# Kernel optimization log

Hardware: AMD Instinct MI355X
Metric: run time of the kernel (lower is better)

Reference implementation:

```python
import jax, jax.numpy as jnp
import numpy as np

B, N, D, H = 4, 2048, 64, 8

def setup_inputs() -> dict:
    key = jax.random.key(0)
    ks = jax.random.split(key, 6)
    s = 0.05
    return {
        "x":  jax.random.normal(ks[0], (B, N, D), dtype=jnp.float32),
        "Wq": jax.random.normal(ks[1], (D, D * H), dtype=jnp.float32) * s,
        "Wk": jax.random.normal(ks[2], (D, D * H), dtype=jnp.float32) * s,
        "Wv": jax.random.normal(ks[3], (D, D * H), dtype=jnp.float32) * s,
        "Wu": jax.random.normal(ks[4], (D * H, D), dtype=jnp.float32) * s,
        "bu": jnp.zeros((D,), dtype=jnp.float32),
    }

def reference(x, Wq, Wk, Wv, Wu, bu):
    b, n, d = x.shape
    h = Wq.shape[1] // d
    # projections: each head has full width d (per the original module)
    q = (x @ Wq).reshape(b, n, h, d).transpose(0, 2, 1, 3)  # [b,h,n,d]
    k = (x @ Wk).reshape(b, n, h, d).transpose(0, 2, 1, 3)
    v = (x @ Wv).reshape(b, n, h, d).transpose(0, 2, 1, 3)
    scores = jnp.einsum('bhnd,bhmd->bhnm', q, k) / jnp.sqrt(jnp.float32(d))
    w = jax.nn.softmax(scores, axis=-1)
    y = jnp.einsum('bhnm,bhmd->bhnd', w, v)          # [b,h,n,d]
    y = y.transpose(0, 2, 1, 3).reshape(b, n, h * d)  # [b,n,h*d]
    return y @ Wu + bu
```

## Files before the change

kernel.cpp:

```cpp
#include <hip/hip_runtime.h>
#include <hip/hip_bf16.h>

#define BB 4
#define NN 2048
#define DD 64
#define HH 8
#define DHH 512

typedef __bf16 bf16_t;
typedef __bf16 bf16x8 __attribute__((ext_vector_type(8)));
typedef __bf16 bf16x4 __attribute__((ext_vector_type(4)));
typedef float f32x4 __attribute__((ext_vector_type(4)));
typedef long long i64;
typedef i64 i64x2 __attribute__((ext_vector_type(2)));
typedef _Float16 f16_t;
typedef _Float16 f16x4 __attribute__((ext_vector_type(4)));
typedef __fp16 h16x2 __attribute__((ext_vector_type(2)));

__device__ __forceinline__ void dma16(const void* g, void* l) {
    __builtin_amdgcn_global_load_lds(
        (const __attribute__((address_space(1))) unsigned int*)g,
        (__attribute__((address_space(3))) unsigned int*)l,
        16, 0, 0);
}

#define MFMA   __builtin_amdgcn_mfma_f32_16x16x32_bf16
#define MFMA8  __builtin_amdgcn_mfma_f32_16x16x32_fp8_fp8
#define MFMA16F __builtin_amdgcn_mfma_f32_16x16x16f16

#define QSCALE 0.18033688011112042f


__global__ __launch_bounds__(256) void prep(
    const float* __restrict__ Wq, const float* __restrict__ Wk,
    const float* __restrict__ Wv, const float* __restrict__ Wu,
    bf16_t* __restrict__ Wqt, bf16_t* __restrict__ Wkt,
    bf16_t* __restrict__ Wvt, bf16_t* __restrict__ Wut)
{
    const int bid = blockIdx.x, tid = threadIdx.x;
    if (bid < 12) {
        const int m = bid >> 2, slice = bid & 3;
        const float* src = (m == 0) ? Wq : (m == 1) ? Wk : Wv;
        bf16_t* dst = (m == 0) ? Wqt : (m == 1) ? Wkt : Wvt;
        const float scale = (m == 0) ? QSCALE : 1.0f;
        const int dc = slice * 128 + (tid >> 1);
        const int kbase = (tid & 1) * 32;
        #pragma unroll
        for (int k0 = 0; k0 < 4; ++k0) {
            bf16x8 p;
            #pragma unroll
            for (int j = 0; j < 8; ++j)
                p[j] = (bf16_t)(src[(size_t)(kbase + k0 * 8 + j) * 512 + dc] * scale);
            *(bf16x8*)(dst + dc * 64 + kbase + k0 * 8) = p;
        }
    } else {
        const int kq = (bid - 12) * 128;
        const int dc = tid >> 2, sub = (tid & 3) * 32;
        #pragma unroll
        for (int k0 = 0; k0 < 4; ++k0) {
            bf16x8 p;
            #pragma unroll
            for (int j = 0; j < 8; ++j)
                p[j] = (bf16_t)Wu[(size_t)(kq + sub + k0 * 8 + j) * 64 + dc];
            *(bf16x8*)(Wut + dc * 512 + kq + sub + k0 * 8) = p;
        }
    }
}

__global__ __launch_bounds__(256) void qkv_mfma(
    const float* __restrict__ x, const bf16_t* __restrict__ Wqt,
    const bf16_t* __restrict__ Wkt, const bf16_t* __restrict__ Wvt,
    char* __restrict__ q8, char* __restrict__ k8, f16_t* __restrict__ vt)
{
    const int n0   = blockIdx.x * 64;
    const int h    = blockIdx.y;
    const int tid  = threadIdx.x;
    const int w    = tid >> 6;
    const int lane = tid & 63;
    const int quad = lane >> 4;
    const int c    = lane & 15;
    const int cq   = c & 7;
    const int l8   = lane >> 3;
    const int lg   = (lane & 7) ^ l8;
    const int lo   = l8 * 128 + lg * 16;
    const int sw0  = ((quad    ) ^ cq) * 16;
    const int sw1  = ((quad + 4) ^ cq) * 16;
    const int w2048 = w * 2048;

    __shared__ __align__(16) float  xs[64 * 64];
    __shared__ __align__(16) bf16_t Wqs[64 * 64], Wks[64 * 64], Wvs[64 * 64];

    {
        const int rloc = lane >> 4;
        const int s    = lane & 15;
        #pragma unroll
        for (int j = 0; j < 4; ++j) {
            int chunk = w * 4 + j;
            int r7 = (chunk * 4 + rloc) & 7;
            const char* src = (const char*)(x + (size_t)(n0 + chunk * 4 + rloc) * 64)
                            + ((s & 8) | ((s & 7) ^ r7)) * 16;
            dma16(src, (char*)xs + chunk * 1024);
        }
    }
    const char* qg = (const char*)Wqt + (size_t)h * 8192;
    const char* kg = (const char*)Wkt + (size_t)h * 8192;
    const char* vg = (const char*)Wvt + (size_t)h * 8192;
    dma16(qg + w2048 + lo,        (char*)Wqs + w2048);
    dma16(qg + w2048 + 1024 + lo, (char*)Wqs + w2048 + 1024);
    dma16(kg + w2048 + lo,        (char*)Wks + w2048);
    dma16(kg + w2048 + 1024 + lo, (char*)Wks + w2048 + 1024);
    dma16(vg + w2048 + lo,        (char*)Wvs + w2048);
    dma16(vg + w2048 + 1024 + lo, (char*)Wvs + w2048 + 1024);
    __syncthreads();

    auto xfrag = [&](int row, int kk) -> bf16x8 {
        const char* rbase = (const char*)xs + row * 256;
        int g0 = kk * 8 + ((quad * 2    ) ^ cq);
        int g1 = kk * 8 + ((quad * 2 + 1) ^ cq);
        f32x4 a = *(const f32x4*)(rbase + g0 * 16);
        f32x4 b = *(const f32x4*)(rbase + g1 * 16);
        bf16x8 r;
        r[0] = (bf16_t)a[0]; r[1] = (bf16_t)a[1]; r[2] = (bf16_t)a[2]; r[3] = (bf16_t)a[3];
        r[4] = (bf16_t)b[0]; r[5] = (bf16_t)b[1]; r[6] = (bf16_t)b[2]; r[7] = (bf16_t)b[3];
        return r;
    };

    bf16x8 xf0 = xfrag(w * 16 + c, 0);
    bf16x8 xf1 = xfrag(w * 16 + c, 1);

    const int gr = n0 + w * 16 + c;
    const int bb = gr >> 11, nn = gr & 2047;
    char* qrow_g = q8 + (((size_t)bb * HH + h) * NN + nn) * 64;
    char* krow_g = k8 + (((size_t)bb * HH + h) * NN + nn) * 64;
    const int nsw = nn & 3;

    #pragma unroll
    for (int mb = 0; mb < 4; ++mb) {
        const char* aq = (const char*)Wqs + (mb * 16 + c) * 128;
        const char* ak = (const char*)Wks + (mb * 16 + c) * 128;
        f32x4 accq = (f32x4){0.f, 0.f, 0.f, 0.f};
        f32x4 acck = (f32x4){0.f, 0.f, 0.f, 0.f};
        accq = MFMA(*(const bf16x8*)(aq + sw0), xf0, accq, 0, 0, 0);
        accq = MFMA(*(const bf16x8*)(aq + sw1), xf1, accq, 0, 0, 0);
        acck = MFMA(*(const bf16x8*)(ak + sw0), xf0, acck, 0, 0, 0);
        acck = MFMA(*(const bf16x8*)(ak + sw1), xf1, acck, 0, 0, 0);
        int g2  = (mb * 2 + (quad >> 1)) & 3;
        int off = ((quad & 1) * 4) + ((mb >> 1) * 8) + ((g2 ^ nsw) * 16);
        int pq = __builtin_amdgcn_cvt_pk_fp8_f32(accq[0], accq[1], 0, false);
        pq     = __builtin_amdgcn_cvt_pk_fp8_f32(accq[2], accq[3], pq, true);
        int pk = __builtin_amdgcn_cvt_pk_fp8_f32(acck[0], acck[1], 0, false);
        pk     = __builtin_amdgcn_cvt_pk_fp8_f32(acck[2], acck[3], pk, true);
        *(int*)(qrow_g + off) = pq;
        *(int*)(krow_g + off) = pk;
    }

    const char* wvrow = (const char*)Wvs + (w * 16 + c) * 128;
    bf16x8 vf0 = *(const bf16x8*)(wvrow + sw0);
    bf16x8 vf1 = *(const bf16x8*)(wvrow + sw1);

    const int bb2 = n0 >> 11;
    f16_t* vtrow_g = vt + (((size_t)bb2 * HH + h) * DD + (w * 16 + c)) * NN + (n0 & 2047);

    #pragma unroll
    for (int nb = 0; nb < 4; ++nb) {
        f32x4 acc = (f32x4){0.f, 0.f, 0.f, 0.f};
        acc = MFMA(xfrag(nb * 16 + c, 0), vf0, acc, 0, 0, 0);
        acc = MFMA(xfrag(nb * 16 + c, 1), vf1, acc, 0, 0, 0);
        f16x4 p = { (f16_t)acc[0], (f16_t)acc[1], (f16_t)acc[2], (f16_t)acc[3] };
        *(f16x4*)(vtrow_g + nb * 16 + quad * 4) = p;
    }
}

__global__ __launch_bounds__(256, 4) void flash_attn(
    const char* __restrict__ q8, const char* __restrict__ k8,
    const f16_t* __restrict__ vt, bf16_t* __restrict__ y)
{
    const int h    = blockIdx.x;
    const int n0   = blockIdx.y * 64;
    const int b    = blockIdx.z;
    const int tid  = threadIdx.x;
    const int w    = tid >> 6;
    const int lane = tid & 63;
    const int quad = lane >> 4;
    const int c    = lane & 15;
    const int ksw  = (quad ^ (c & 3)) * 16;

    __shared__ __align__(16) char LB[17408];

    const size_t bh = (size_t)(b * HH + h);
    const char* qp = q8 + bh * (size_t)(NN * 64);
    const char* kp = k8 + bh * (size_t)(NN * 64);
    const char* vp = (const char*)(vt + bh * (size_t)(DD * NN));

    i64x2 qf[4];
    #pragma unroll
    for (int cb = 0; cb < 4; ++cb)
        qf[cb] = *(const i64x2*)(qp + (size_t)(n0 + cb * 16 + c) * 64 + ksw);

    const char* kfp = kp + (size_t)(w * 16 + c) * 64 + ksw;
    const char* vfp = vp + (size_t)c * 4096 + w * 32 + quad * 8;

    i64x2 kf = *(const i64x2*)(kfp);
    f16x4 vf[4];
    #pragma unroll
    for (int db = 0; db < 4; ++db)
        vf[db] = *(const f16x4*)(vfp + db * 65536);

    float lsum[4] = {0.f, 0.f, 0.f, 0.f};
    f32x4 o[4][4];
    #pragma unroll
    for (int db = 0; db < 4; ++db)
        #pragma unroll
        for (int cb = 0; cb < 4; ++cb) o[db][cb] = (f32x4){0.f, 0.f, 0.f, 0.f};

    for (int kt = 0; kt < 32; ++kt) {
        const int kt2 = (kt + 1) & 31;
        i64x2 kf_n = *(const i64x2*)(kfp + (size_t)kt2 * 4096);
        f16x4 vf_n[4];
        #pragma unroll
        for (int db = 0; db < 4; ++db)
            vf_n[db] = *(const f16x4*)(vfp + db * 65536 + (size_t)kt2 * 128);

        #pragma unroll
        for (int cb = 0; cb < 4; ++cb) {
            f32x4 s = (f32x4){0.f, 0.f, 0.f, 0.f};
            s = MFMA8(kf.x, qf[cb].x, s, 0, 0, 0);
            s = MFMA8(kf.y, qf[cb].y, s, 0, 0, 0);
            float p0 = __builtin_amdgcn_exp2f(s[0]);
            float p1 = __builtin_amdgcn_exp2f(s[1]);
            float p2 = __builtin_amdgcn_exp2f(s[2]);
            float p3 = __builtin_amdgcn_exp2f(s[3]);
            lsum[cb] += (p0 + p1) + (p2 + p3);
            h16x2 ab = __builtin_amdgcn_cvt_pkrtz(p0, p1);
            h16x2 cd = __builtin_amdgcn_cvt_pkrtz(p2, p3);
            f16x4 pf = { (f16_t)ab[0], (f16_t)ab[1], (f16_t)cd[0], (f16_t)cd[1] };
            #pragma unroll
            for (int db = 0; db < 4; ++db)
                o[db][cb] = MFMA16F(vf[db], pf, o[db][cb], 0, 0, 0);
        }

        kf = kf_n;
        #pragma unroll
        for (int db = 0; db < 4; ++db) vf[db] = vf_n[db];
    }

    char* Ob = LB;
    float* Lb = (float*)(LB + 16384);

    #pragma unroll
    for (int cb = 0; cb < 4; ++cb) {
        lsum[cb] += __shfl_xor(lsum[cb], 16, 64);
        lsum[cb] += __shfl_xor(lsum[cb], 32, 64);
    }
    if (quad == 0) {
        #pragma unroll
        for (int cb = 0; cb < 4; ++cb)
            Lb[(w * 4 + cb) * 16 + c] = lsum[cb];
    }

    #pragma unroll
    for (int ww = 0; ww < 4; ++ww) {
        if (w == ww) {
            #pragma unroll
            for (int db = 0; db < 4; ++db) {
                #pragma unroll
                for (int cb = 0; cb < 4; ++cb) {
                    char* p = Ob + (size_t)(((db * 4 + cb) * 4 + quad) * 16 + c) * 16;
                    f32x4 v = o[db][cb];
                    if (ww > 0) v += *(const f32x4*)p;
                    *(f32x4*)p = v;
                }
            }
        }
        __syncthreads();
    }

    {
        const int n_loc = tid & 63;
        const int dq    = tid >> 6;
        const int qcb   = n_loc >> 4;
        const int cc    = n_loc & 15;
        float l = Lb[(0 * 4 + qcb) * 16 + cc] + Lb[(1 * 4 + qcb) * 16 + cc]
                + Lb[(2 * 4 + qcb) * 16 + cc] + Lb[(3 * 4 + qcb) * 16 + cc];
        float inv = 1.0f / l;
        float vals[16];
        #pragma unroll
        for (int q2 = 0; q2 < 4; ++q2) {
            f32x4 v = *(const f32x4*)(Ob
                    + (size_t)(((dq * 4 + qcb) * 4 + q2) * 16 + cc) * 16);
            vals[q2 * 4 + 0] = v[0]; vals[q2 * 4 + 1] = v[1];
            vals[q2 * 4 + 2] = v[2]; vals[q2 * 4 + 3] = v[3];
        }
        bf16x8 o0, o1;
        #pragma unroll
        for (int j = 0; j < 8; ++j) {
            o0[j] = (bf16_t)(vals[j] * inv);
            o1[j] = (bf16_t)(vals[8 + j] * inv);
        }
        bf16_t* yrow = y + bh * (size_t)(NN * DD) + (size_t)(n0 + n_loc) * DD + dq * 16;
        *(bf16x8*)(yrow)     = o0;
        *(bf16x8*)(yrow + 8) = o1;
    }
}

__global__ __launch_bounds__(256) void out_proj(
    const bf16_t* __restrict__ y,
    const bf16_t* __restrict__ Wut,
    const float* __restrict__ bu, float* __restrict__ out)
{
    const int rt   = blockIdx.x >> 1;
    const int dh   = blockIdx.x & 1;
    const int row0 = rt * 32;
    const int b    = row0 >> 11;
    const int nn0  = row0 & 2047;
    const int tid  = threadIdx.x;
    const int w    = tid >> 6;
    const int lane = tid & 63;
    const int quad = lane >> 4;
    const int c    = lane & 15;
    const int cq   = c & 7;

    __shared__ __align__(16) bf16_t ys[32 * 512];

    {
        const int hsel = lane >> 3;
        const int g7   = lane & 7;
        #pragma unroll
        for (int rr = 0; rr < 8; ++rr) {
            int row = w * 8 + rr;
            const char* src = (const char*)y
                + (((size_t)b * HH + hsel) * NN + nn0 + row) * 128
                + ((g7 ^ (row & 7)) * 16);
            dma16(src, (char*)ys + row * 1024);
        }
    }
    __syncthreads();

    const int rows16 = (w >> 1) * 16;
    const int mb     = dh * 2 + (w & 1);
    const char* yrow = (const char*)ys + (rows16 + c) * 1024;

    f32x4 acc = (f32x4){0.f, 0.f, 0.f, 0.f};
    #pragma unroll
    for (int kk = 0; kk < 16; ++kk) {
        int g = kk * 4 + quad;
        bf16x8 bfrag = *(const bf16x8*)(yrow + (((g & ~7) | ((g & 7) ^ cq)) * 16));
        bf16x8 afrag = *(const bf16x8*)((const char*)Wut
                        + (size_t)(mb * 16 + c) * 1024 + kk * 64 + quad * 16);
        acc = MFMA(afrag, bfrag, acc, 0, 0, 0);
    }

    float4 bb = *(const float4*)(bu + mb * 16 + quad * 4);
    float4 res = { acc[0] + bb.x, acc[1] + bb.y, acc[2] + bb.z, acc[3] + bb.w };
    float* op = out + (size_t)(row0 + rows16 + c) * DD + mb * 16 + quad * 4;
    *(float4*)op = res;
}

extern "C" void kernel_launch(void* const* d_in, const int* in_sizes, int n_in,
                              void* d_out, int out_size, void* d_ws, size_t ws_size,
                              hipStream_t stream) {
    const float* x  = (const float*)d_in[0];
    const float* Wq = (const float*)d_in[1];
    const float* Wk = (const float*)d_in[2];
    const float* Wv = (const float*)d_in[3];
    const float* Wu = (const float*)d_in[4];
    const float* bu = (const float*)d_in[5];
    float* out = (float*)d_out;

    const size_t SEG8 = (size_t)BB * HH * NN * 64;
    const size_t SEG  = SEG8 * 2;
    char* ws = (char*)d_ws;
    char*   q8  = ws;
    char*   k8  = ws + SEG8;
    f16_t*  vt  = (f16_t*)(ws + 2 * SEG8);
    bf16_t* y   = (bf16_t*)(ws + 2 * SEG8 + SEG);
    bf16_t* Wqt = (bf16_t*)(ws + 2 * SEG8 + 2 * SEG);
    bf16_t* Wkt = (bf16_t*)(ws + 2 * SEG8 + 2 * SEG + (1 << 16));
    bf16_t* Wvt = (bf16_t*)(ws + 2 * SEG8 + 2 * SEG + 2 * (1 << 16));
    bf16_t* Wut = (bf16_t*)(ws + 2 * SEG8 + 2 * SEG + 3 * (1 << 16));

    prep<<<dim3(16), dim3(256), 0, stream>>>(Wq, Wk, Wv, Wu, Wqt, Wkt, Wvt, Wut);
    qkv_mfma<<<dim3(128, 8), dim3(256), 0, stream>>>(x, Wqt, Wkt, Wvt, q8, k8, vt);
    flash_attn<<<dim3(HH, NN / 64, BB), dim3(256), 0, stream>>>(q8, k8, vt, y);
    out_proj<<<dim3(512), dim3(256), 0, stream>>>(y, Wut, bu, out);
}
```

Before: 156.2 us.

## Stage K/V tiles through LDS via async global_load_lds double buffering

The flash attention loop stops loading K and V fragments straight from global memory into registers with a one-step register prefetch. Instead it uses global_load_lds DMA into double-buffered shared memory with XOR-swizzled layouts, and each wave reads its fragments from LDS. This aims to coalesce global loads and overlap the next tile's fetch with compute. In exchange it adds a __syncthreads per iteration, grows LDS to 24KB (which may reduce occupancy at 4 blocks/CU), and adds LDS read traffic.

```diff
diff --git a/kernel.cpp b/kernel.cpp
--- a/kernel.cpp
+++ b/kernel.cpp
@@ -183,9 +183,11 @@
     const int lane = tid & 63;
     const int quad = lane >> 4;
     const int c    = lane & 15;
+    const int l8   = lane >> 3;
+    const int lg   = (lane & 7) ^ l8;
     const int ksw  = (quad ^ (c & 3)) * 16;
 
-    __shared__ __align__(16) char LB[17408];
+    __shared__ __align__(16) char SM[24576];
 
     const size_t bh = (size_t)(b * HH + h);
     const char* qp = q8 + bh * (size_t)(NN * 64);
@@ -197,14 +199,14 @@
     for (int cb = 0; cb < 4; ++cb)
         qf[cb] = *(const i64x2*)(qp + (size_t)(n0 + cb * 16 + c) * 64 + ksw);
 
-    const char* kfp = kp + (size_t)(w * 16 + c) * 64 + ksw;
-    const char* vfp = vp + (size_t)c * 4096 + w * 32 + quad * 8;
-
-    i64x2 kf = *(const i64x2*)(kfp);
-    f16x4 vf[4];
-    #pragma unroll
-    for (int db = 0; db < 4; ++db)
-        vf[db] = *(const f16x4*)(vfp + db * 65536);
+    const char* kdma = kp + w * 1024 + lane * 16;
+    const char* vdma = vp + (size_t)(w * 16 + l8) * 4096 + lg * 16;
+    const int kro = (w * 16 + c) * 64 + ksw;
+    const int vro = c * 128 + (((w * 2 + (quad >> 1)) ^ (c & 7)) * 16) + (quad & 1) * 8;
+
+    dma16(kdma,          SM + w * 1024);
+    dma16(vdma,          SM + 8192 + w * 2048);
+    dma16(vdma + 32768,  SM + 8192 + w * 2048 + 1024);
 
     float lsum[4] = {0.f, 0.f, 0.f, 0.f};
     f32x4 o[4][4];
@@ -213,13 +215,31 @@
         #pragma unroll
         for (int cb = 0; cb < 4; ++cb) o[db][cb] = (f32x4){0.f, 0.f, 0.f, 0.f};
 
+    __syncthreads();
+
+    dma16(kdma + 4096,          SM + 4096 + w * 1024);
+    dma16(vdma + 128,           SM + 16384 + w * 2048);
+    dma16(vdma + 128 + 32768,   SM + 16384 + w * 2048 + 1024);
+
     for (int kt = 0; kt < 32; ++kt) {
-        const int kt2 = (kt + 1) & 31;
-        i64x2 kf_n = *(const i64x2*)(kfp + (size_t)kt2 * 4096);
-        f16x4 vf_n[4];
+        const int buf = kt & 1;
+        if (kt > 0) {
+            __syncthreads();
+            if (kt < 31) {
+                const size_t adv = (size_t)(kt + 1);
+                dma16(kdma + adv * 4096,         SM + (buf ^ 1) * 4096 + w * 1024);
+                dma16(vdma + adv * 128,          SM + 8192 + (buf ^ 1) * 8192 + w * 2048);
+                dma16(vdma + adv * 128 + 32768,  SM + 8192 + (buf ^ 1) * 8192 + w * 2048 + 1024);
+            }
+        }
+        const char* kb = SM + buf * 4096;
+        const char* vb = SM + 8192 + buf * 8192;
+
+        i64x2 kf = *(const i64x2*)(kb + kro);
+        f16x4 vf[4];
         #pragma unroll
         for (int db = 0; db < 4; ++db)
-            vf_n[db] = *(const f16x4*)(vfp + db * 65536 + (size_t)kt2 * 128);
+            vf[db] = *(const f16x4*)(vb + vro + db * 2048);
 
         #pragma unroll
         for (int cb = 0; cb < 4; ++cb) {
@@ -238,14 +258,12 @@
             for (int db = 0; db < 4; ++db)
                 o[db][cb] = MFMA16F(vf[db], pf, o[db][cb], 0, 0, 0);
         }
-
-        kf = kf_n;
-        #pragma unroll
-        for (int db = 0; db < 4; ++db) vf[db] = vf_n[db];
-    }
-
-    char* Ob = LB;
-    float* Lb = (float*)(LB + 16384);
+    }
+
+    __syncthreads();
+
+    char*  Ob = SM;
+    float* Lb = (float*)(SM + 16384);
 
     #pragma unroll
     for (int cb = 0; cb < 4; ++cb) {
```

New measurement: 129.0 us. 1.21x faster.
